# Kernel optimization log

Hardware: AMD Instinct MI355X
Metric: run time of the kernel (lower is better)

## Reference

```python
import jax, jax.numpy as jnp
import numpy as np

D_MODEL = 512
D_FF = 2048
D_K = 64
N_HEADS = 8
LN_EPS = 1e-5


def layer_norm(x, gamma, beta):
    mu = jnp.mean(x, axis=-1, keepdims=True)
    var = jnp.mean(jnp.square(x - mu), axis=-1, keepdims=True)
    return (x - mu) * jax.lax.rsqrt(var + LN_EPS) * gamma + beta


def setup_inputs() -> dict:
    key = jax.random.key(0)
    ks = jax.random.split(key, 8)
    B, S = 16, 1024
    s_in = 1.0 / np.sqrt(D_MODEL)
    s_ff = 1.0 / np.sqrt(D_FF)
    return {
        "x": jax.random.normal(ks[0], (B, S, D_MODEL), jnp.float32),
        # shared QKV projection (the module uses ONE linear for Q, K and V)
        "w_qkv": jax.random.uniform(ks[1], (D_MODEL, D_MODEL), jnp.float32, -s_in, s_in),
        "b_qkv": jnp.zeros((D_MODEL,), jnp.float32),
        "w_out": jax.random.uniform(ks[2], (D_MODEL, D_MODEL), jnp.float32, -s_in, s_in),
        "b_out": jnp.zeros((D_MODEL,), jnp.float32),
        "w1": jax.random.uniform(ks[3], (D_FF, D_MODEL), jnp.float32, -s_in, s_in),
        "b1": jnp.zeros((D_FF,), jnp.float32),
        "w2": jax.random.uniform(ks[4], (D_MODEL, D_FF), jnp.float32, -s_ff, s_ff),
        "b2": jnp.zeros((D_MODEL,), jnp.float32),
        "g1": jnp.ones((D_MODEL,), jnp.float32),
        "be1": jnp.zeros((D_MODEL,), jnp.float32),
        "g2": jnp.ones((D_MODEL,), jnp.float32),
        "be2": jnp.zeros((D_MODEL,), jnp.float32),
    }


def reference(x, w_qkv, b_qkv, w_out, b_out, w1, b1, w2, b2, g1, be1, g2, be2):
    B, S, _ = x.shape
    # --- MultiHeadAttention (shared linear for Q/K/V, dropout = identity) ---
    qkv = x @ w_qkv.T + b_qkv                       # [B,S,D]
    h = qkv.reshape(B, S, N_HEADS, D_K)             # Q = K = V
    scores = jnp.einsum("bqhd,bkhd->bhqk", h, h) / np.sqrt(D_K)
    probs = jax.nn.softmax(scores, axis=-1)
    ctx = jnp.einsum("bhqk,bkhd->bqhd", probs, h).reshape(B, S, D_MODEL)
    attn = ctx @ w_out.T + b_out
    # --- dual-LayerNorm residual #1: x = norm1(x) + norm1(attn) ---
    x = layer_norm(x, g1, be1) + layer_norm(attn, g1, be1)
    # --- FFN ---
    ffn = jax.nn.relu(x @ w1.T + b1) @ w2.T + b2
    # --- residual #2: x = x + norm2(ffn) ---
    return x + layer_norm(ffn, g2, be2)
```

## Files before the change

kernel.cpp:

```cpp
#include <hip/hip_runtime.h>
#include <hip/hip_bf16.h>
#include <stdint.h>


using bf16 = __bf16;
typedef __attribute__((ext_vector_type(2))) __bf16 bf16x2;
typedef __attribute__((ext_vector_type(4))) __bf16 bf16x4;
typedef __attribute__((ext_vector_type(8))) __bf16 bf16x8;
typedef __attribute__((ext_vector_type(4))) float floatx4;
typedef __attribute__((ext_vector_type(16))) float f32x16;

#define AS1 __attribute__((address_space(1)))
#define AS3 __attribute__((address_space(3)))

#define L2E 1.44269504088896340736f

constexpr int BN_ = 16, SQ_ = 1024, DM_ = 512, DFF_ = 2048, NH_ = 8, DK_ = 64;
constexpr int ROWS_ = BN_ * SQ_;

__device__ __forceinline__ void f2b_one(const float* __restrict__ in,
                                        bf16* __restrict__ out, int i) {
  float4 a = ((const float4*)in)[2 * i];
  float4 b = ((const float4*)in)[2 * i + 1];
  bf16x8 o;
  o[0] = (bf16)a.x; o[1] = (bf16)a.y; o[2] = (bf16)a.z; o[3] = (bf16)a.w;
  o[4] = (bf16)b.x; o[5] = (bf16)b.y; o[6] = (bf16)b.z; o[7] = (bf16)b.w;
  ((bf16x8*)out)[i] = o;
}

__global__ __launch_bounds__(256) void f2b5_kernel(
    const float* __restrict__ s0, bf16* __restrict__ d0, int n0,
    const float* __restrict__ s1, bf16* __restrict__ d1, int n1,
    const float* __restrict__ s2, bf16* __restrict__ d2, int n2,
    const float* __restrict__ s3, bf16* __restrict__ d3, int n3,
    const float* __restrict__ s4, bf16* __restrict__ d4, int n4) {
  int i = blockIdx.x * 256 + threadIdx.x;
  if (i < n0) { f2b_one(s0, d0, i); return; }  i -= n0;
  if (i < n1) { f2b_one(s1, d1, i); return; }  i -= n1;
  if (i < n2) { f2b_one(s2, d2, i); return; }  i -= n2;
  if (i < n3) { f2b_one(s3, d3, i); return; }  i -= n3;
  if (i < n4) { f2b_one(s4, d4, i); }
}

template <int RELU>
__global__ __launch_bounds__(256) void gemm_bt(const bf16* __restrict__ A,
                                               const bf16* __restrict__ B,
                                               const float* __restrict__ bias,
                                               bf16* __restrict__ C,
                                               int M, int N, int K) {
  __shared__ char glds[32768];
  const int tid = threadIdx.x;
  const int lane = tid & 63;
  const int wv = tid >> 6;
  const int wr = wv >> 1, wc = wv & 1;
  const int r15 = lane & 15, g = lane >> 4;
  const int tileN = blockIdx.x * 128;
  const int tileM = blockIdx.y * 128;

  floatx4 acc[4][4] = {};

  uint32_t dstoff[2];
  const bf16* srcA[2];
  const bf16* srcB[2];
#pragma unroll
  for (int is = 0; is < 2; ++is) {
    const int base = wv * 2048 + is * 1024;
    const int ob = base + lane * 16;
    const int row = ob >> 6;
    const int pslot = (ob >> 4) & 3;
    const int sslot = pslot ^ ((row >> 1) & 3);
    dstoff[is] = base;
    srcA[is] = A + (size_t)(tileM + row) * K + sslot * 8;
    srcB[is] = B + (size_t)(tileN + row) * K + sslot * 8;
  }

#define GSTAGE(buf, kt)                                                         \
  {                                                                             \
    _Pragma("unroll")                                                           \
    for (int is = 0; is < 2; ++is) {                                            \
      __builtin_amdgcn_global_load_lds(                                         \
          (AS1 uint32_t*)(srcA[is] + (kt) * 32),                                \
          (AS3 uint32_t*)((AS3 char*)glds + (buf) * 8192 + dstoff[is]), 16, 0, 0); \
      __builtin_amdgcn_global_load_lds(                                         \
          (AS1 uint32_t*)(srcB[is] + (kt) * 32),                                \
          (AS3 uint32_t*)((AS3 char*)glds + 16384 + (buf) * 8192 + dstoff[is]), \
          16, 0, 0);                                                            \
    }                                                                           \
  }

  uint32_t aoff[4], boff[4];
#pragma unroll
  for (int m = 0; m < 4; ++m) {
    const int arow = wr * 64 + m * 16 + r15;
    aoff[m] = (uint32_t)((arow * 64 + g * 16) ^ (((arow >> 1) & 3) << 4));
  }
#pragma unroll
  for (int n = 0; n < 4; ++n) {
    const int brow = wc * 64 + n * 16 + r15;
    boff[n] = (uint32_t)((brow * 64 + g * 16) ^ (((brow >> 1) & 3) << 4));
  }

  const int nk = K >> 5;
  GSTAGE(0, 0);

  for (int kt = 0; kt < nk; ++kt) {
    const int cur = kt & 1;
    if (kt + 1 < nk) {
      GSTAGE(cur ^ 1, kt + 1);
      asm volatile("s_waitcnt vmcnt(4)" ::: "memory");
    } else {
      asm volatile("s_waitcnt vmcnt(0)" ::: "memory");
    }
    __builtin_amdgcn_s_barrier();
    __builtin_amdgcn_sched_barrier(0);

    const char* Ac = (const char*)glds + cur * 8192;
    const char* Bc = (const char*)glds + 16384 + cur * 8192;

    bf16x8 af[4], bfr[4];
#pragma unroll
    for (int m = 0; m < 4; ++m) af[m] = *(const bf16x8*)(Ac + aoff[m]);
#pragma unroll
    for (int n = 0; n < 4; ++n) bfr[n] = *(const bf16x8*)(Bc + boff[n]);
#pragma unroll
    for (int m = 0; m < 4; ++m)
#pragma unroll
      for (int n = 0; n < 4; ++n)
        acc[m][n] = __builtin_amdgcn_mfma_f32_16x16x32_bf16(af[m], bfr[n],
                                                            acc[m][n], 0, 0, 0);
    __builtin_amdgcn_s_barrier();
  }
#undef GSTAGE

#pragma unroll
  for (int n = 0; n < 4; ++n) {
    const int col = tileN + wc * 64 + n * 16 + r15;
    const float bv = bias[col];
#pragma unroll
    for (int m = 0; m < 4; ++m) {
      const int row0 = tileM + wr * 64 + m * 16 + g * 4;
#pragma unroll
      for (int j = 0; j < 4; ++j) {
        float v = acc[m][n][j] + bv;
        if (RELU) v = fmaxf(v, 0.f);
        C[(size_t)(row0 + j) * N + col] = (bf16)v;
      }
    }
  }
}

template <int RELU>
__global__ __launch_bounds__(256) void gemm_bt64(const bf16* __restrict__ A,
                                                 const bf16* __restrict__ B,
                                                 const float* __restrict__ bias,
                                                 bf16* __restrict__ C,
                                                 int M, int N, int K) {
  __shared__ char glds[65536];
  const int tid = threadIdx.x;
  const int lane = tid & 63;
  const int wv = tid >> 6;
  const int wr = wv >> 1, wc = wv & 1;
  const int r15 = lane & 15, g = lane >> 4;
  const int tileN = blockIdx.x * 128;
  const int tileM = blockIdx.y * 128;

  floatx4 acc[4][4] = {};

  uint32_t dstoff[4];
  const bf16* srcA[4];
  const bf16* srcB[4];
#pragma unroll
  for (int is = 0; is < 4; ++is) {
    const int base = is * 4096 + wv * 1024;
    const int ob = base + lane * 16;
    const int row = ob >> 7;
    const int pslot = (ob >> 4) & 7;
    const int sslot = pslot ^ (row & 7);
    dstoff[is] = base;
    srcA[is] = A + (size_t)(tileM + row) * K + sslot * 8;
    srcB[is] = B + (size_t)(tileN + row) * K + sslot * 8;
  }

#define GSTAGE64(buf, kt)                                                        \
  {                                                                              \
    _Pragma("unroll")                                                            \
    for (int is = 0; is < 4; ++is) {                                             \
      __builtin_amdgcn_global_load_lds(                                          \
          (AS1 uint32_t*)(srcA[is] + (kt) * 64),                                 \
          (AS3 uint32_t*)((AS3 char*)glds + (buf) * 16384 + dstoff[is]), 16, 0, 0); \
      __builtin_amdgcn_global_load_lds(                                          \
          (AS1 uint32_t*)(srcB[is] + (kt) * 64),                                 \
          (AS3 uint32_t*)((AS3 char*)glds + 32768 + (buf) * 16384 + dstoff[is]), \
          16, 0, 0);                                                             \
    }                                                                            \
  }

  uint32_t abase[4], ax[4], bbase[4], bx[4];
#pragma unroll
  for (int m = 0; m < 4; ++m) {
    const int arow = wr * 64 + m * 16 + r15;
    abase[m] = (uint32_t)(arow * 128);
    ax[m] = (uint32_t)(arow & 7);
  }
#pragma unroll
  for (int n = 0; n < 4; ++n) {
    const int brow = wc * 64 + n * 16 + r15;
    bbase[n] = (uint32_t)(brow * 128);
    bx[n] = (uint32_t)(brow & 7);
  }

  const int nk = K >> 6;
  GSTAGE64(0, 0);

  for (int kt = 0; kt < nk; ++kt) {
    const int cur = kt & 1;
    if (kt + 1 < nk) {
      GSTAGE64(cur ^ 1, kt + 1);
      asm volatile("s_waitcnt vmcnt(8)" ::: "memory");
    } else {
      asm volatile("s_waitcnt vmcnt(0)" ::: "memory");
    }
    __builtin_amdgcn_s_barrier();
    __builtin_amdgcn_sched_barrier(0);

    const char* Ac = (const char*)glds + cur * 16384;
    const char* Bc = (const char*)glds + 32768 + cur * 16384;

#pragma unroll
    for (int kk = 0; kk < 2; ++kk) {
      bf16x8 af[4], bfr[4];
#pragma unroll
      for (int m = 0; m < 4; ++m) {
        const uint32_t slot = (uint32_t)(kk * 4 + g) ^ ax[m];
        af[m] = *(const bf16x8*)(Ac + abase[m] + slot * 16);
      }
#pragma unroll
      for (int n = 0; n < 4; ++n) {
        const uint32_t slot = (uint32_t)(kk * 4 + g) ^ bx[n];
        bfr[n] = *(const bf16x8*)(Bc + bbase[n] + slot * 16);
      }
#pragma unroll
      for (int m = 0; m < 4; ++m)
#pragma unroll
        for (int n = 0; n < 4; ++n)
          acc[m][n] = __builtin_amdgcn_mfma_f32_16x16x32_bf16(af[m], bfr[n],
                                                              acc[m][n], 0, 0, 0);
    }
    __builtin_amdgcn_s_barrier();
  }
#undef GSTAGE64

#pragma unroll
  for (int n = 0; n < 4; ++n) {
    const int col = tileN + wc * 64 + n * 16 + r15;
    const float bv = bias[col];
#pragma unroll
    for (int m = 0; m < 4; ++m) {
      const int row0 = tileM + wr * 64 + m * 16 + g * 4;
#pragma unroll
      for (int j = 0; j < 4; ++j) {
        float v = acc[m][n][j] + bv;
        if (RELU) v = fmaxf(v, 0.f);
        C[(size_t)(row0 + j) * N + col] = (bf16)v;
      }
    }
  }
}

__global__ __launch_bounds__(256) void attn_kernel(const bf16* __restrict__ qkv,
                                                   bf16* __restrict__ ctx) {
  __shared__ char lds[32768];

  const int tid = threadIdx.x;
  const int lane = tid & 63;
  const int wv = tid >> 6;
  const int l31 = lane & 31;
  const int h = lane >> 5;
  const int b = blockIdx.z, hd = blockIdx.y, qt = blockIdx.x;
  const size_t headoff = (size_t)b * SQ_ * DM_ + hd * DK_;
  const int q0 = qt * 128 + wv * 32;

  const float QS = 0.125f * L2E;
  bf16x8 aq[4];
#pragma unroll
  for (int kd = 0; kd < 4; ++kd) {
    const bf16* gq = qkv + headoff + (size_t)(q0 + l31) * DM_ + kd * 16 + h * 8;
    bf16x8 v = *(const bf16x8*)gq;
#pragma unroll
    for (int e = 0; e < 8; ++e) v[e] = (bf16)((float)v[e] * QS);
    aq[kd] = v;
  }

  f32x16 o0 = {}, o1 = {};
  float mstate = -1e30f, lstate = 0.f;

  const uint32_t ldsb = (uint32_t)(uintptr_t)(AS3 char*)lds;

  uint32_t dstoff[4];
  const bf16* srcb[4];
#pragma unroll
  for (int is = 0; is < 4; ++is) {
    const int ob = is * 4096 + wv * 1024 + lane * 16;
    const int e0 = ob >> 1;
    const int srow = ((e0 >> 8) << 2) + ((e0 >> 4) & 3);
    const int dcol = ((e0 >> 6) & 3) * 16 + ((e0 >> 3) & 1) * 8;
    dstoff[is] = is * 4096 + wv * 1024;
    srcb[is] = qkv + headoff + (size_t)srow * DM_ + dcol;
  }

#define STAGE(buf, t)                                                          \
  {                                                                            \
    _Pragma("unroll")                                                          \
    for (int is = 0; is < 4; ++is) {                                           \
      __builtin_amdgcn_global_load_lds(                                        \
          (AS1 uint32_t*)(srcb[is] + (size_t)(t) * 128 * DM_),                 \
          (AS3 uint32_t*)((AS3 char*)lds + (buf) * 16384 + dstoff[is]), 16, 0, 0); \
    }                                                                          \
  }

  constexpr int NT = SQ_ / 128;
  STAGE(0, 0);

  for (int t = 0; t < NT; ++t) {
    const int cur = t & 1;
    __builtin_amdgcn_s_barrier();
    if (t + 1 < NT) {
      STAGE(cur ^ 1, t + 1);
      asm volatile("s_waitcnt vmcnt(4)" ::: "memory");
    } else {
      asm volatile("s_waitcnt vmcnt(0)" ::: "memory");
    }
    __builtin_amdgcn_s_barrier();
    __builtin_amdgcn_sched_barrier(0);

#pragma unroll
    for (int p = 0; p < 2; ++p) {
      const char* tile = (const char*)lds + cur * 16384 + p * 8192;

      f32x16 s0v = {}, s1v = {};
      const char* pabase = tile + (l31 >> 2) * 512 + (l31 & 3) * 32 + h * 16;
      __builtin_amdgcn_s_setprio(1);
#pragma unroll
      for (int kd = 0; kd < 4; ++kd) {
        bf16x8 a0 = *(const bf16x8*)(pabase + kd * 128);
        bf16x8 a1 = *(const bf16x8*)(pabase + kd * 128 + 4096);
        s0v = __builtin_amdgcn_mfma_f32_32x32x16_bf16(a0, aq[kd], s0v, 0, 0, 0);
        s1v = __builtin_amdgcn_mfma_f32_32x32x16_bf16(a1, aq[kd], s1v, 0, 0, 0);
      }
      __builtin_amdgcn_s_setprio(0);

      float mx = s0v[0];
#pragma unroll
      for (int r = 1; r < 16; ++r) mx = fmaxf(mx, s0v[r]);
#pragma unroll
      for (int r = 0; r < 16; ++r) mx = fmaxf(mx, s1v[r]);
      mx = fmaxf(mx, __shfl_xor(mx, 32));
      if (!__all(mx - mstate <= 8.f)) {
        const float nm = fmaxf(mstate, mx);
        const float al = exp2f(mstate - nm);
        mstate = nm;
        lstate *= al;
#pragma unroll
        for (int r = 0; r < 16; ++r) { o0[r] *= al; o1[r] *= al; }
      }
      float rs = 0.f;
#pragma unroll
      for (int r = 0; r < 16; ++r) {
        float pq = exp2f(s0v[r] - mstate);
        s0v[r] = pq; rs += pq;
      }
#pragma unroll
      for (int r = 0; r < 16; ++r) {
        float pq = exp2f(s1v[r] - mstate);
        s1v[r] = pq; rs += pq;
      }
      rs += __shfl_xor(rs, 32);
      lstate += rs;

      uint32_t pf[4][4];
#pragma unroll
      for (int ks = 0; ks < 4; ++ks) {
        const int kb = (ks & 1) * 8;
        float v0, v1, v2, v3, v4, v5, v6, v7;
        if (ks < 2) {
          v0 = s0v[kb+0]; v1 = s0v[kb+1]; v2 = s0v[kb+2]; v3 = s0v[kb+3];
          v4 = s0v[kb+4]; v5 = s0v[kb+5]; v6 = s0v[kb+6]; v7 = s0v[kb+7];
        } else {
          v0 = s1v[kb+0]; v1 = s1v[kb+1]; v2 = s1v[kb+2]; v3 = s1v[kb+3];
          v4 = s1v[kb+4]; v5 = s1v[kb+5]; v6 = s1v[kb+6]; v7 = s1v[kb+7];
        }
        union { bf16x2 v; uint32_t u; } P0, P1, P2, P3;
        P0.v = bf16x2{(bf16)v0, (bf16)v1};
        P1.v = bf16x2{(bf16)v2, (bf16)v3};
        P2.v = bf16x2{(bf16)v4, (bf16)v5};
        P3.v = bf16x2{(bf16)v6, (bf16)v7};
        asm volatile("v_permlane32_swap_b32 %0, %1" : "+v"(P0.u), "+v"(P2.u));
        asm volatile("v_permlane32_swap_b32 %0, %1" : "+v"(P1.u), "+v"(P3.u));
        pf[ks][0] = P0.u;
        pf[ks][1] = P1.u;
        pf[ks][2] = P2.u;
        pf[ks][3] = P3.u;
      }

#pragma unroll
      for (int df = 0; df < 2; ++df) {
        const uint32_t vb = ldsb + cur * 16384 + p * 8192 + df * 256 +
                            (lane & 15) * 8 + ((lane >> 4) & 1) * 128 +
                            (lane >> 5) * 1024;
        bf16x4 lo[4], hi[4];
#pragma unroll
        for (int ks = 0; ks < 4; ++ks) {
          asm volatile("ds_read_b64_tr_b16 %0, %2\n\t"
                       "ds_read_b64_tr_b16 %1, %2 offset:512"
                       : "=&v"(lo[ks]), "=&v"(hi[ks])
                       : "v"(vb + ks * 2048));
        }
        asm volatile("s_waitcnt lgkmcnt(0)" ::: "memory");
        __builtin_amdgcn_sched_barrier(0);
        __builtin_amdgcn_s_setprio(1);
#pragma unroll
        for (int ks = 0; ks < 4; ++ks) {
          union { struct { bf16x4 l, h; } pp; bf16x8 v; } av;
          av.pp.l = lo[ks]; av.pp.h = hi[ks];
          union { uint32_t u[4]; bf16x8 v; } bv;
          bv.u[0] = pf[ks][0]; bv.u[1] = pf[ks][1];
          bv.u[2] = pf[ks][2]; bv.u[3] = pf[ks][3];
          if (df == 0)
            o0 = __builtin_amdgcn_mfma_f32_32x32x16_bf16(av.v, bv.v, o0, 0, 0, 0);
          else
            o1 = __builtin_amdgcn_mfma_f32_32x32x16_bf16(av.v, bv.v, o1, 0, 0, 0);
        }
        __builtin_amdgcn_s_setprio(0);
      }
    }
  }
#undef STAGE

  __syncthreads();
  const float invl = 1.f / lstate;
  char* wb = (char*)lds + wv * 4096;
#pragma unroll
  for (int df = 0; df < 2; ++df)
#pragma unroll
    for (int t = 0; t < 4; ++t) {
      const f32x16& ov = df ? o1 : o0;
      bf16x4 pkt;
      pkt[0] = (bf16)(ov[4*t+0] * invl);
      pkt[1] = (bf16)(ov[4*t+1] * invl);
      pkt[2] = (bf16)(ov[4*t+2] * invl);
      pkt[3] = (bf16)(ov[4*t+3] * invl);
      const int byte = (l31 * 128 + df * 64 + t * 16 + h * 8) ^ ((l31 & 7) << 4);
      *(bf16x4*)(wb + byte) = pkt;
    }
#pragma unroll
  for (int ps = 0; ps < 4; ++ps) {
    const int qr = ps * 8 + (lane >> 3);
    const int byte = (qr * 128 + (lane & 7) * 16) ^ ((qr & 7) << 4);
    bf16x8 vv = *(const bf16x8*)(wb + byte);
    bf16* dst = ctx + (size_t)(b * SQ_ + q0 + qr) * DM_ + hd * 64 + (lane & 7) * 8;
    *(bf16x8*)dst = vv;
  }
}

__global__ __launch_bounds__(256) void dual_ln_kernel(const bf16* __restrict__ x,
                                                      const bf16* __restrict__ attn,
                                                      const float* __restrict__ g1,
                                                      const float* __restrict__ be1,
                                                      bf16* __restrict__ out) {
  const int row = blockIdx.x * 4 + (threadIdx.x >> 6);
  const int lane = threadIdx.x & 63;
  bf16x8 xv = *(const bf16x8*)(x + (size_t)row * DM_ + lane * 8);
  bf16x8 av = *(const bf16x8*)(attn + (size_t)row * DM_ + lane * 8);
  float xs[8], as_[8];
#pragma unroll
  for (int e = 0; e < 8; ++e) { xs[e] = (float)xv[e]; as_[e] = (float)av[e]; }
  float sx = 0, sx2 = 0, sa = 0, sa2 = 0;
#pragma unroll
  for (int e = 0; e < 8; ++e) {
    sx += xs[e]; sx2 += xs[e] * xs[e];
    sa += as_[e]; sa2 += as_[e] * as_[e];
  }
#pragma unroll
  for (int off = 1; off < 64; off <<= 1) {
    sx += __shfl_xor(sx, off);  sx2 += __shfl_xor(sx2, off);
    sa += __shfl_xor(sa, off);  sa2 += __shfl_xor(sa2, off);
  }
  const float inv = 1.f / (float)DM_;
  const float mux = sx * inv, mua = sa * inv;
  const float rx = rsqrtf(fmaxf(sx2 * inv - mux * mux, 0.f) + 1e-5f);
  const float ra = rsqrtf(fmaxf(sa2 * inv - mua * mua, 0.f) + 1e-5f);
  bf16x8 ov;
#pragma unroll
  for (int e = 0; e < 8; ++e) {
    const int c = lane * 8 + e;
    const float val = ((xs[e] - mux) * rx + (as_[e] - mua) * ra) * g1[c] + 2.f * be1[c];
    ov[e] = (bf16)val;
  }
  *(bf16x8*)(out + (size_t)row * DM_ + lane * 8) = ov;
}

__global__ __launch_bounds__(256) void final_ln_kernel(const bf16* __restrict__ x1,
                                                       const bf16* __restrict__ ffn,
                                                       const float* __restrict__ g2,
                                                       const float* __restrict__ be2,
                                                       float* __restrict__ out) {
  const int row = blockIdx.x * 4 + (threadIdx.x >> 6);
  const int lane = threadIdx.x & 63;
  bf16x8 xv = *(const bf16x8*)(x1 + (size_t)row * DM_ + lane * 8);
  bf16x8 fv = *(const bf16x8*)(ffn + (size_t)row * DM_ + lane * 8);
  float fs[8];
#pragma unroll
  for (int e = 0; e < 8; ++e) fs[e] = (float)fv[e];
  float sf = 0, sf2 = 0;
#pragma unroll
  for (int e = 0; e < 8; ++e) { sf += fs[e]; sf2 += fs[e] * fs[e]; }
#pragma unroll
  for (int off = 1; off < 64; off <<= 1) {
    sf += __shfl_xor(sf, off);  sf2 += __shfl_xor(sf2, off);
  }
  const float inv = 1.f / (float)DM_;
  const float mu = sf * inv;
  const float rs = rsqrtf(fmaxf(sf2 * inv - mu * mu, 0.f) + 1e-5f);
  float ov[8];
#pragma unroll
  for (int e = 0; e < 8; ++e) {
    const int c = lane * 8 + e;
    ov[e] = (float)xv[e] + (fs[e] - mu) * rs * g2[c] + be2[c];
  }
  float* orow = out + (size_t)row * DM_ + lane * 8;
  float4 o0 = {ov[0], ov[1], ov[2], ov[3]};
  float4 o1 = {ov[4], ov[5], ov[6], ov[7]};
  ((float4*)orow)[0] = o0;
  ((float4*)orow)[1] = o1;
}

extern "C" void kernel_launch(void* const* d_in, const int* in_sizes, int n_in,
                              void* d_out, int out_size, void* d_ws, size_t ws_size,
                              hipStream_t stream) {
  const float* x     = (const float*)d_in[0];
  const float* w_qkv = (const float*)d_in[1];
  const float* b_qkv = (const float*)d_in[2];
  const float* w_out = (const float*)d_in[3];
  const float* b_out = (const float*)d_in[4];
  const float* w1    = (const float*)d_in[5];
  const float* b1    = (const float*)d_in[6];
  const float* w2    = (const float*)d_in[7];
  const float* b2    = (const float*)d_in[8];
  const float* g1    = (const float*)d_in[9];
  const float* be1   = (const float*)d_in[10];
  const float* g2    = (const float*)d_in[11];
  const float* be2   = (const float*)d_in[12];
  float* out = (float*)d_out;

  char* ws = (char*)d_ws;
  const size_t o_wqkv = 0;
  const size_t o_wout = o_wqkv + (size_t)DM_ * DM_ * 2;
  const size_t o_w1   = o_wout + (size_t)DM_ * DM_ * 2;
  const size_t o_w2   = o_w1 + (size_t)DFF_ * DM_ * 2;
  const size_t o_A    = o_w2 + (size_t)DM_ * DFF_ * 2;
  const size_t o_B    = o_A + (size_t)ROWS_ * DM_ * 2;
  const size_t o_C    = o_B + (size_t)ROWS_ * DM_ * 2;
  const size_t o_D    = o_C + (size_t)ROWS_ * DM_ * 2;
  const size_t need   = o_D + (size_t)ROWS_ * DFF_ * 2;
  if (ws_size < need) return;

  bf16* wqkv_bf = (bf16*)(ws + o_wqkv);
  bf16* wout_bf = (bf16*)(ws + o_wout);
  bf16* w1_bf   = (bf16*)(ws + o_w1);
  bf16* w2_bf   = (bf16*)(ws + o_w2);
  bf16* bufA    = (bf16*)(ws + o_A);
  bf16* bufB    = (bf16*)(ws + o_B);
  bf16* bufC    = (bf16*)(ws + o_C);
  bf16* bufD    = (bf16*)(ws + o_D);

  const int nx  = ROWS_ * DM_ / 8;
  const int nwq = DM_ * DM_ / 8;
  const int nw1 = DFF_ * DM_ / 8;
  const int ntot = nx + 2 * nwq + 2 * nw1;
  f2b5_kernel<<<dim3((ntot + 255) / 256), dim3(256), 0, stream>>>(
      x, bufD, nx,
      w_qkv, wqkv_bf, nwq,
      w_out, wout_bf, nwq,
      w1, w1_bf, nw1,
      w2, w2_bf, nw1);

  gemm_bt64<0><<<dim3(DM_ / 128, ROWS_ / 128), dim3(256), 0, stream>>>(bufD, wqkv_bf, b_qkv, bufB, ROWS_, DM_, DM_);

  attn_kernel<<<dim3(SQ_ / 128, NH_, BN_), dim3(256), 0, stream>>>(bufB, bufA);

  gemm_bt64<0><<<dim3(DM_ / 128, ROWS_ / 128), dim3(256), 0, stream>>>(bufA, wout_bf, b_out, bufC, ROWS_, DM_, DM_);

  dual_ln_kernel<<<dim3(ROWS_ / 4), dim3(256), 0, stream>>>(bufD, bufC, g1, be1, bufB);

  gemm_bt<1><<<dim3(DFF_ / 128, ROWS_ / 128), dim3(256), 0, stream>>>(bufB, w1_bf, b1, bufD, ROWS_, DFF_, DM_);

  gemm_bt64<0><<<dim3(DM_ / 128, ROWS_ / 128), dim3(256), 0, stream>>>(bufD, w2_bf, b2, bufC, ROWS_, DM_, DFF_);

  final_ln_kernel<<<dim3(ROWS_ / 4), dim3(256), 0, stream>>>(bufB, bufC, g2, be2, out);
}
```

Before: 229.1 us.

## Split attention key range across two wave groups and merge softmax states

The attention kernel now launches 512 threads per block. Two groups of four waves each process half of the key sequence with their own double-buffered LDS tiles. At the end, group 1 writes its partial output, max and sum to LDS, and group 0 merges them using the online-softmax rescaling before writing ctx. This halves the serial key loop per wave to expose more parallelism and latency hiding. The cost is extra LDS use, a merge step with additional barriers, and possibly lower occupancy from the larger block.

Result: no change. 227.5 us (-0.7%).

```diff
diff --git a/kernel.cpp b/kernel.cpp
--- a/kernel.cpp
+++ b/kernel.cpp
@@ -267,18 +267,21 @@
   }
 }
 
-__global__ __launch_bounds__(256) void attn_kernel(const bf16* __restrict__ qkv,
+__global__ __launch_bounds__(512) void attn_kernel(const bf16* __restrict__ qkv,
                                                    bf16* __restrict__ ctx) {
-  __shared__ char lds[32768];
+  __shared__ char lds[34816];
 
   const int tid = threadIdx.x;
   const int lane = tid & 63;
   const int wv = tid >> 6;
+  const int wq = wv & 3;
+  const int grp = wv >> 2;
   const int l31 = lane & 31;
   const int h = lane >> 5;
   const int b = blockIdx.z, hd = blockIdx.y, qt = blockIdx.x;
   const size_t headoff = (size_t)b * SQ_ * DM_ + hd * DK_;
-  const int q0 = qt * 128 + wv * 32;
+  const int q0 = qt * 128 + wq * 32;
+  const int go = grp * 512;
 
   const float QS = 0.125f * L2E;
   bf16x8 aq[4];
@@ -296,29 +299,29 @@
 
   const uint32_t ldsb = (uint32_t)(uintptr_t)(AS3 char*)lds;
 
-  uint32_t dstoff[4];
-  const bf16* srcb[4];
-#pragma unroll
-  for (int is = 0; is < 4; ++is) {
-    const int ob = is * 4096 + wv * 1024 + lane * 16;
+  uint32_t dstoff[2];
+  const bf16* srcb[2];
+#pragma unroll
+  for (int is = 0; is < 2; ++is) {
+    const int ob = is * 4096 + wq * 1024 + lane * 16;
     const int e0 = ob >> 1;
     const int srow = ((e0 >> 8) << 2) + ((e0 >> 4) & 3);
     const int dcol = ((e0 >> 6) & 3) * 16 + ((e0 >> 3) & 1) * 8;
-    dstoff[is] = is * 4096 + wv * 1024;
-    srcb[is] = qkv + headoff + (size_t)srow * DM_ + dcol;
+    dstoff[is] = (uint32_t)(grp * 16384 + is * 4096 + wq * 1024);
+    srcb[is] = qkv + headoff + (size_t)(go + srow) * DM_ + dcol;
   }
 
 #define STAGE(buf, t)                                                          \
   {                                                                            \
     _Pragma("unroll")                                                          \
-    for (int is = 0; is < 4; ++is) {                                           \
+    for (int is = 0; is < 2; ++is) {                                           \
       __builtin_amdgcn_global_load_lds(                                        \
-          (AS1 uint32_t*)(srcb[is] + (size_t)(t) * 128 * DM_),                 \
-          (AS3 uint32_t*)((AS3 char*)lds + (buf) * 16384 + dstoff[is]), 16, 0, 0); \
+          (AS1 uint32_t*)(srcb[is] + (size_t)(t) * 64 * DM_),                  \
+          (AS3 uint32_t*)((AS3 char*)lds + (buf) * 8192 + dstoff[is]), 16, 0, 0); \
     }                                                                          \
   }
 
-  constexpr int NT = SQ_ / 128;
+  constexpr int NT = 512 / 64;
   STAGE(0, 0);
 
   for (int t = 0; t < NT; ++t) {
@@ -326,139 +329,163 @@
     __builtin_amdgcn_s_barrier();
     if (t + 1 < NT) {
       STAGE(cur ^ 1, t + 1);
-      asm volatile("s_waitcnt vmcnt(4)" ::: "memory");
+      asm volatile("s_waitcnt vmcnt(2)" ::: "memory");
     } else {
       asm volatile("s_waitcnt vmcnt(0)" ::: "memory");
     }
     __builtin_amdgcn_s_barrier();
     __builtin_amdgcn_sched_barrier(0);
 
-#pragma unroll
-    for (int p = 0; p < 2; ++p) {
-      const char* tile = (const char*)lds + cur * 16384 + p * 8192;
-
-      f32x16 s0v = {}, s1v = {};
-      const char* pabase = tile + (l31 >> 2) * 512 + (l31 & 3) * 32 + h * 16;
+    const char* tile = (const char*)lds + grp * 16384 + cur * 8192;
+
+    f32x16 s0v = {}, s1v = {};
+    const char* pabase = tile + (l31 >> 2) * 512 + (l31 & 3) * 32 + h * 16;
+    __builtin_amdgcn_s_setprio(1);
+#pragma unroll
+    for (int kd = 0; kd < 4; ++kd) {
+      bf16x8 a0 = *(const bf16x8*)(pabase + kd * 128);
+      bf16x8 a1 = *(const bf16x8*)(pabase + kd * 128 + 4096);
+      s0v = __builtin_amdgcn_mfma_f32_32x32x16_bf16(a0, aq[kd], s0v, 0, 0, 0);
+      s1v = __builtin_amdgcn_mfma_f32_32x32x16_bf16(a1, aq[kd], s1v, 0, 0, 0);
+    }
+    __builtin_amdgcn_s_setprio(0);
+
+    float mx = s0v[0];
+#pragma unroll
+    for (int r = 1; r < 16; ++r) mx = fmaxf(mx, s0v[r]);
+#pragma unroll
+    for (int r = 0; r < 16; ++r) mx = fmaxf(mx, s1v[r]);
+    mx = fmaxf(mx, __shfl_xor(mx, 32));
+    if (!__all(mx - mstate <= 8.f)) {
+      const float nm = fmaxf(mstate, mx);
+      const float al = exp2f(mstate - nm);
+      mstate = nm;
+      lstate *= al;
+#pragma unroll
+      for (int r = 0; r < 16; ++r) { o0[r] *= al; o1[r] *= al; }
+    }
+    float rs = 0.f;
+#pragma unroll
+    for (int r = 0; r < 16; ++r) {
+      float pq = exp2f(s0v[r] - mstate);
+      s0v[r] = pq; rs += pq;
+    }
+#pragma unroll
+    for (int r = 0; r < 16; ++r) {
+      float pq = exp2f(s1v[r] - mstate);
+      s1v[r] = pq; rs += pq;
+    }
+    rs += __shfl_xor(rs, 32);
+    lstate += rs;
+
+    uint32_t pf[4][4];
+#pragma unroll
+    for (int ks = 0; ks < 4; ++ks) {
+      const int kb = (ks & 1) * 8;
+      float v0, v1, v2, v3, v4, v5, v6, v7;
+      if (ks < 2) {
+        v0 = s0v[kb+0]; v1 = s0v[kb+1]; v2 = s0v[kb+2]; v3 = s0v[kb+3];
+        v4 = s0v[kb+4]; v5 = s0v[kb+5]; v6 = s0v[kb+6]; v7 = s0v[kb+7];
+      } else {
+        v0 = s1v[kb+0]; v1 = s1v[kb+1]; v2 = s1v[kb+2]; v3 = s1v[kb+3];
+        v4 = s1v[kb+4]; v5 = s1v[kb+5]; v6 = s1v[kb+6]; v7 = s1v[kb+7];
+      }
+      union { bf16x2 v; uint32_t u; } P0, P1, P2, P3;
+      P0.v = bf16x2{(bf16)v0, (bf16)v1};
+      P1.v = bf16x2{(bf16)v2, (bf16)v3};
+      P2.v = bf16x2{(bf16)v4, (bf16)v5};
+      P3.v = bf16x2{(bf16)v6, (bf16)v7};
+      asm volatile("v_permlane32_swap_b32 %0, %1" : "+v"(P0.u), "+v"(P2.u));
+      asm volatile("v_permlane32_swap_b32 %0, %1" : "+v"(P1.u), "+v"(P3.u));
+      pf[ks][0] = P0.u;
+      pf[ks][1] = P1.u;
+      pf[ks][2] = P2.u;
+      pf[ks][3] = P3.u;
+    }
+
+#pragma unroll
+    for (int df = 0; df < 2; ++df) {
+      const uint32_t vb = ldsb + grp * 16384 + cur * 8192 + df * 256 +
+                          (lane & 15) * 8 + ((lane >> 4) & 1) * 128 +
+                          (lane >> 5) * 1024;
+      bf16x4 lo[4], hi[4];
+#pragma unroll
+      for (int ks = 0; ks < 4; ++ks) {
+        asm volatile("ds_read_b64_tr_b16 %0, %2\n\t"
+                     "ds_read_b64_tr_b16 %1, %2 offset:512"
+                     : "=&v"(lo[ks]), "=&v"(hi[ks])
+                     : "v"(vb + ks * 2048));
+      }
+      asm volatile("s_waitcnt lgkmcnt(0)" ::: "memory");
+      __builtin_amdgcn_sched_barrier(0);
       __builtin_amdgcn_s_setprio(1);
 #pragma unroll
-      for (int kd = 0; kd < 4; ++kd) {
-        bf16x8 a0 = *(const bf16x8*)(pabase + kd * 128);
-        bf16x8 a1 = *(const bf16x8*)(pabase + kd * 128 + 4096);
-        s0v = __builtin_amdgcn_mfma_f32_32x32x16_bf16(a0, aq[kd], s0v, 0, 0, 0);
-        s1v = __builtin_amdgcn_mfma_f32_32x32x16_bf16(a1, aq[kd], s1v, 0, 0, 0);
+      for (int ks = 0; ks < 4; ++ks) {
+        union { struct { bf16x4 l, h; } pp; bf16x8 v; } av;
+        av.pp.l = lo[ks]; av.pp.h = hi[ks];
+        union { uint32_t u[4]; bf16x8 v; } bv;
+        bv.u[0] = pf[ks][0]; bv.u[1] = pf[ks][1];
+        bv.u[2] = pf[ks][2]; bv.u[3] = pf[ks][3];
+        if (df == 0)
+          o0 = __builtin_amdgcn_mfma_f32_32x32x16_bf16(av.v, bv.v, o0, 0, 0, 0);
+        else
+          o1 = __builtin_amdgcn_mfma_f32_32x32x16_bf16(av.v, bv.v, o1, 0, 0, 0);
       }
       __builtin_amdgcn_s_setprio(0);
-
-      float mx = s0v[0];
-#pragma unroll
-      for (int r = 1; r < 16; ++r) mx = fmaxf(mx, s0v[r]);
-#pragma unroll
-      for (int r = 0; r < 16; ++r) mx = fmaxf(mx, s1v[r]);
-      mx = fmaxf(mx, __shfl_xor(mx, 32));
-      if (!__all(mx - mstate <= 8.f)) {
-        const float nm = fmaxf(mstate, mx);
-        const float al = exp2f(mstate - nm);
-        mstate = nm;
-        lstate *= al;
-#pragma unroll
-        for (int r = 0; r < 16; ++r) { o0[r] *= al; o1[r] *= al; }
-      }
-      float rs = 0.f;
-#pragma unroll
-      for (int r = 0; r < 16; ++r) {
-        float pq = exp2f(s0v[r] - mstate);
-        s0v[r] = pq; rs += pq;
-      }
-#pragma unroll
-      for (int r = 0; r < 16; ++r) {
-        float pq = exp2f(s1v[r] - mstate);
-        s1v[r] = pq; rs += pq;
-      }
-      rs += __shfl_xor(rs, 32);
-      lstate += rs;
-
-      uint32_t pf[4][4];
-#pragma unroll
-      for (int ks = 0; ks < 4; ++ks) {
-        const int kb = (ks & 1) * 8;
-        float v0, v1, v2, v3, v4, v5, v6, v7;
-        if (ks < 2) {
-          v0 = s0v[kb+0]; v1 = s0v[kb+1]; v2 = s0v[kb+2]; v3 = s0v[kb+3];
-          v4 = s0v[kb+4]; v5 = s0v[kb+5]; v6 = s0v[kb+6]; v7 = s0v[kb+7];
-        } else {
-          v0 = s1v[kb+0]; v1 = s1v[kb+1]; v2 = s1v[kb+2]; v3 = s1v[kb+3];
-          v4 = s1v[kb+4]; v5 = s1v[kb+5]; v6 = s1v[kb+6]; v7 = s1v[kb+7];
-        }
-        union { bf16x2 v; uint32_t u; } P0, P1, P2, P3;
-        P0.v = bf16x2{(bf16)v0, (bf16)v1};
-        P1.v = bf16x2{(bf16)v2, (bf16)v3};
-        P2.v = bf16x2{(bf16)v4, (bf16)v5};
-        P3.v = bf16x2{(bf16)v6, (bf16)v7};
-        asm volatile("v_permlane32_swap_b32 %0, %1" : "+v"(P0.u), "+v"(P2.u));
-        asm volatile("v_permlane32_swap_b32 %0, %1" : "+v"(P1.u), "+v"(P3.u));
-        pf[ks][0] = P0.u;
-        pf[ks][1] = P1.u;
-        pf[ks][2] = P2.u;
-        pf[ks][3] = P3.u;
-      }
-
-#pragma unroll
-      for (int df = 0; df < 2; ++df) {
-        const uint32_t vb = ldsb + cur * 16384 + p * 8192 + df * 256 +
-                            (lane & 15) * 8 + ((lane >> 4) & 1) * 128 +
-                            (lane >> 5) * 1024;
-        bf16x4 lo[4], hi[4];
-#pragma unroll
-        for (int ks = 0; ks < 4; ++ks) {
-          asm volatile("ds_read_b64_tr_b16 %0, %2\n\t"
-                       "ds_read_b64_tr_b16 %1, %2 offset:512"
-                       : "=&v"(lo[ks]), "=&v"(hi[ks])
-                       : "v"(vb + ks * 2048));
-        }
-        asm volatile("s_waitcnt lgkmcnt(0)" ::: "memory");
-        __builtin_amdgcn_sched_barrier(0);
-        __builtin_amdgcn_s_setprio(1);
-#pragma unroll
-        for (int ks = 0; ks < 4; ++ks) {
-          union { struct { bf16x4 l, h; } pp; bf16x8 v; } av;
-          av.pp.l = lo[ks]; av.pp.h = hi[ks];
-          union { uint32_t u[4]; bf16x8 v; } bv;
-          bv.u[0] = pf[ks][0]; bv.u[1] = pf[ks][1];
-          bv.u[2] = pf[ks][2]; bv.u[3] = pf[ks][3];
-          if (df == 0)
-            o0 = __builtin_amdgcn_mfma_f32_32x32x16_bf16(av.v, bv.v, o0, 0, 0, 0);
-          else
-            o1 = __builtin_amdgcn_mfma_f32_32x32x16_bf16(av.v, bv.v, o1, 0, 0, 0);
-        }
-        __builtin_amdgcn_s_setprio(0);
-      }
     }
   }
 #undef STAGE
 
   __syncthreads();
-  const float invl = 1.f / lstate;
-  char* wb = (char*)lds + wv * 4096;
-#pragma unroll
-  for (int df = 0; df < 2; ++df)
-#pragma unroll
-    for (int t = 0; t < 4; ++t) {
-      const f32x16& ov = df ? o1 : o0;
-      bf16x4 pkt;
-      pkt[0] = (bf16)(ov[4*t+0] * invl);
-      pkt[1] = (bf16)(ov[4*t+1] * invl);
-      pkt[2] = (bf16)(ov[4*t+2] * invl);
-      pkt[3] = (bf16)(ov[4*t+3] * invl);
-      const int byte = (l31 * 128 + df * 64 + t * 16 + h * 8) ^ ((l31 & 7) << 4);
-      *(bf16x4*)(wb + byte) = pkt;
-    }
-#pragma unroll
-  for (int ps = 0; ps < 4; ++ps) {
-    const int qr = ps * 8 + (lane >> 3);
-    const int byte = (qr * 128 + (lane & 7) * 16) ^ ((qr & 7) << 4);
-    bf16x8 vv = *(const bf16x8*)(wb + byte);
-    bf16* dst = ctx + (size_t)(b * SQ_ + q0 + qr) * DM_ + hd * 64 + (lane & 7) * 8;
-    *(bf16x8*)dst = vv;
+  if (grp == 1) {
+    float* dst = (float*)((char*)lds + wq * 8192) + lane * 32;
+#pragma unroll
+    for (int r = 0; r < 16; ++r) { dst[r] = o0[r]; dst[16 + r] = o1[r]; }
+    float2* ml = (float2*)((char*)lds + 32768 + wq * 512 + lane * 8);
+    *ml = float2{mstate, lstate};
+  }
+  __syncthreads();
+  if (grp == 0) {
+    const float* src = (const float*)((char*)lds + wq * 8192) + lane * 32;
+    const float2 ml = *(const float2*)((const char*)lds + 32768 + wq * 512 + lane * 8);
+    const float mB = ml.x, lB = ml.y;
+    const float m = fmaxf(mstate, mB);
+    const float fa = exp2f(mstate - m);
+    const float fb = exp2f(mB - m);
+    lstate = lstate * fa + lB * fb;
+#pragma unroll
+    for (int r = 0; r < 16; ++r) {
+      o0[r] = o0[r] * fa + src[r] * fb;
+      o1[r] = o1[r] * fa + src[16 + r] * fb;
+    }
+    mstate = m;
+  }
+  __syncthreads();
+
+  if (grp == 0) {
+    const float invl = 1.f / lstate;
+    char* wb = (char*)lds + wq * 4096;
+#pragma unroll
+    for (int df = 0; df < 2; ++df)
+#pragma unroll
+      for (int t = 0; t < 4; ++t) {
+        const f32x16& ov = df ? o1 : o0;
+        bf16x4 pkt;
+        pkt[0] = (bf16)(ov[4*t+0] * invl);
+        pkt[1] = (bf16)(ov[4*t+1] * invl);
+        pkt[2] = (bf16)(ov[4*t+2] * invl);
+        pkt[3] = (bf16)(ov[4*t+3] * invl);
+        const int byte = (l31 * 128 + df * 64 + t * 16 + h * 8) ^ ((l31 & 7) << 4);
+        *(bf16x4*)(wb + byte) = pkt;
+      }
+#pragma unroll
+    for (int ps = 0; ps < 4; ++ps) {
+      const int qr = ps * 8 + (lane >> 3);
+      const int byte = (qr * 128 + (lane & 7) * 16) ^ ((qr & 7) << 4);
+      bf16x8 vv = *(const bf16x8*)(wb + byte);
+      bf16* dst = ctx + (size_t)(b * SQ_ + q0 + qr) * DM_ + hd * 64 + (lane & 7) * 8;
+      *(bf16x8*)dst = vv;
+    }
   }
 }
 
@@ -586,7 +613,7 @@
 
   gemm_bt64<0><<<dim3(DM_ / 128, ROWS_ / 128), dim3(256), 0, stream>>>(bufD, wqkv_bf, b_qkv, bufB, ROWS_, DM_, DM_);
 
-  attn_kernel<<<dim3(SQ_ / 128, NH_, BN_), dim3(256), 0, stream>>>(bufB, bufA);
+  attn_kernel<<<dim3(SQ_ / 128, NH_, BN_), dim3(512), 0, stream>>>(bufB, bufA);
 
   gemm_bt64<0><<<dim3(DM_ / 128, ROWS_ / 128), dim3(256), 0, stream>>>(bufA, wout_bf, b_out, bufC, ROWS_, DM_, DM_);
 
```
